# Kernel tuning notes

Hardware: AMD Instinct MI355X
Metric: run time of the kernel (lower is better)

Reference implementation:

```python
import jax, jax.numpy as jnp
import numpy as np

NUM_HEAD = 8
EMBED_DIM = 512


def setup_inputs() -> dict:
    key = jax.random.key(0)
    ks = jax.random.split(key, 9)
    B, N, D = 4, 2048, 512
    # xavier_uniform bound for square [D, D] weights
    bound = float(np.sqrt(6.0 / (D + EMBED_DIM)))
    return {
        "q": jax.random.normal(ks[0], (B, N, D), jnp.float32),
        "k": jax.random.normal(ks[1], (B, N, D), jnp.float32),
        "v": jax.random.normal(ks[2], (B, N, D), jnp.float32),
        "Wq": jax.random.uniform(ks[3], (D, EMBED_DIM), jnp.float32, -bound, bound),
        "Wk": jax.random.uniform(ks[4], (D, EMBED_DIM), jnp.float32, -bound, bound),
        "Wv": jax.random.uniform(ks[5], (D, EMBED_DIM), jnp.float32, -bound, bound),
        "bq": jnp.zeros((EMBED_DIM,), jnp.float32),
        "bk": jnp.zeros((EMBED_DIM,), jnp.float32),
        "bv": jnp.zeros((EMBED_DIM,), jnp.float32),
    }


def reference(q, k, v, Wq, Wk, Wv, bq, bk, bv):
    h = NUM_HEAD
    ch = EMBED_DIM // h
    B, N, _ = q.shape
    # linear projections
    Q = q @ Wq + bq  # [B, N, E]
    K = k @ Wk + bk
    V = v @ Wv + bv
    # split heads: b n (h ch) -> b h n ch
    Q = Q.reshape(B, N, h, ch).transpose(0, 2, 1, 3)
    K = K.reshape(B, N, h, ch).transpose(0, 2, 1, 3)
    V = V.reshape(B, N, h, ch).transpose(0, 2, 1, 3)
    scale = 1.0 / np.sqrt(ch).astype(np.float32)
    scores = jnp.einsum("bhqc,bhkc->bhqk", Q, K) * scale  # [B, h, N, N]
    attn = jax.nn.softmax(scores, axis=-1)
    out = jnp.einsum("bhqk,bhkc->bhqc", attn, V)  # [B, h, N, ch]
    # merge heads: b h n ch -> b n (h ch)
    return out.transpose(0, 2, 1, 3).reshape(B, N, EMBED_DIM)
```

## Files before the change

### kernel.cpp

```cpp
#include <hip/hip_runtime.h>
#include <hip/hip_bf16.h>
#include <cstdint>

#define B_ 4
#define N_ 2048
#define D_ 512
#define E_ 512
#define H_ 8
#define CH_ 64
#define M_ (B_*N_)

typedef __attribute__((ext_vector_type(8))) short bf16x8;
typedef __attribute__((ext_vector_type(4))) float f32x4;
typedef __attribute__((ext_vector_type(16))) float f32x16;
using u16 = unsigned short;
using u32 = unsigned int;

__device__ __forceinline__ u16 f2bf(float f) {
  union { __hip_bfloat16 h; u16 u; } cv;
  cv.h = __float2bfloat16(f);
  return cv.u;
}

__device__ __forceinline__ float fexp2(float x) {
#if __has_builtin(__builtin_amdgcn_exp2f)
  return __builtin_amdgcn_exp2f(x);
#else
  return exp2f(x);
#endif
}

__device__ __forceinline__ void async16(const void* g, void* l) {
  __builtin_amdgcn_global_load_lds(
      (__attribute__((address_space(1))) void*)(g),
      (__attribute__((address_space(3))) void*)(l),
      16, 0, 0);
}

__global__ void prep_w(const float* __restrict__ Wq, const float* __restrict__ Wk,
                       const float* __restrict__ Wv,
                       u16* __restrict__ tq, u16* __restrict__ tk, u16* __restrict__ tv) {
  int bid = blockIdx.x;
  int t = bid >> 10;
  const float* W = (t == 0) ? Wq : (t == 1 ? Wk : Wv);
  u16* T = (t == 0) ? tq : (t == 1 ? tk : tv);
  int idx = ((bid & 1023) << 8) + threadIdx.x;
  int e = idx >> 9, kd = idx & 511;
  T[idx] = f2bf(W[kd * E_ + e]);
}

#define GBM 128
#define GBN 128
#define GBK 64

__global__ __launch_bounds__(256) void proj_gemm(
    const float* __restrict__ xq, const float* __restrict__ xk, const float* __restrict__ xv,
    const u16* __restrict__ wtq, const u16* __restrict__ wtk, const u16* __restrict__ wtv,
    const float* __restrict__ bq, const float* __restrict__ bk, const float* __restrict__ bv,
    u16* __restrict__ Qp, u16* __restrict__ Kp, u16* __restrict__ Vp) {
  const int z = blockIdx.z;
  const float* X = (z == 0) ? xq : (z == 1 ? xk : xv);
  const u16* WT  = (z == 0) ? wtq : (z == 1 ? wtk : wtv);
  const float* bias = (z == 0) ? bq : (z == 1 ? bk : bv);
  u16* Out = (z == 0) ? Qp : (z == 1 ? Kp : Vp);
  const float scale = (z == 0) ? 0.18033688011112042f : 1.0f;
  const bool vlayout = (z == 2);

  __shared__ __align__(16) u16 As[GBM * GBK];
  __shared__ __align__(16) u16 Bs[GBN * GBK];

  const int tid = threadIdx.x;
  const int l = tid & 63, w = tid >> 6;
  const int wr = w >> 1, wc = w & 1;
  const int m0 = blockIdx.y * GBM;
  const int e0 = blockIdx.x * GBN;

  f32x4 acc[4][4] = {};

  for (int ks = 0; ks < D_ / GBK; ++ks) {
    const int k0 = ks * GBK;
#pragma unroll
    for (int i = 0; i < 4; ++i) {
      int o = i * 4096 + tid * 16;
      int row = o >> 7, colb = o & 127;
      int scol = colb ^ ((row & 7) << 4);
      async16((const char*)WT + ((size_t)(e0 + row) * D_ + k0) * 2 + scol, (char*)Bs + o);
    }
    float4 fa[4], fb_[4];
#pragma unroll
    for (int i = 0; i < 4; ++i) {
      int o = i * 4096 + tid * 16;
      int row = o >> 7, colb = o & 127;
      const char* src = (const char*)X + ((size_t)(m0 + row) * D_ + k0) * 4 + colb * 2;
      fa[i]  = *reinterpret_cast<const float4*>(src);
      fb_[i] = *reinterpret_cast<const float4*>(src + 16);
    }
#pragma unroll
    for (int i = 0; i < 4; ++i) {
      int o = i * 4096 + tid * 16;
      int row = o >> 7;
      union { u16 us[8]; bf16x8 v8; } cu;
      cu.us[0] = f2bf(fa[i].x); cu.us[1] = f2bf(fa[i].y);
      cu.us[2] = f2bf(fa[i].z); cu.us[3] = f2bf(fa[i].w);
      cu.us[4] = f2bf(fb_[i].x); cu.us[5] = f2bf(fb_[i].y);
      cu.us[6] = f2bf(fb_[i].z); cu.us[7] = f2bf(fb_[i].w);
      *reinterpret_cast<bf16x8*>((char*)As + (o ^ ((row & 7) << 4))) = cu.v8;
    }
    __syncthreads();
#pragma unroll
    for (int kk = 0; kk < 2; ++kk) {
      bf16x8 af[4], bfr[4];
#pragma unroll
      for (int m = 0; m < 4; ++m) {
        int row = wr * 64 + m * 16 + (l & 15);
        int addr = (row << 7) + kk * 64 + ((l >> 4) << 4);
        addr ^= (row & 7) << 4;
        af[m] = *reinterpret_cast<const bf16x8*>((const char*)As + addr);
      }
#pragma unroll
      for (int n = 0; n < 4; ++n) {
        int row = wc * 64 + n * 16 + (l & 15);
        int addr = (row << 7) + kk * 64 + ((l >> 4) << 4);
        addr ^= (row & 7) << 4;
        bfr[n] = *reinterpret_cast<const bf16x8*>((const char*)Bs + addr);
      }
#pragma unroll
      for (int m = 0; m < 4; ++m)
#pragma unroll
        for (int n = 0; n < 4; ++n)
          acc[m][n] = __builtin_amdgcn_mfma_f32_16x16x32_bf16(af[m], bfr[n], acc[m][n], 0, 0, 0);
    }
    __syncthreads();
  }

#pragma unroll
  for (int m = 0; m < 4; ++m) {
#pragma unroll
    for (int n = 0; n < 4; ++n) {
      int ge = e0 + wc * 64 + n * 16 + (l & 15);
      int h = ge >> 6, c = ge & 63;
      float bv_ = bias[ge];
      int gm0 = m0 + wr * 64 + m * 16 + ((l >> 4) << 2);
      int b = gm0 >> 11, nn0 = gm0 & 2047;
      if (vlayout) {
        short4 sv;
#pragma unroll
        for (int j = 0; j < 4; ++j)
          ((u16*)&sv)[j] = f2bf((acc[m][n][j] + bv_) * scale);
        int np = (((nn0 >> 2) ^ (nn0 >> 3)) & 1) ? (nn0 ^ 12) : nn0;
        *reinterpret_cast<short4*>(
            &Out[(((size_t)b * H_ + h) * CH_ + c) * N_ + np]) = sv;
      } else {
#pragma unroll
        for (int j = 0; j < 4; ++j) {
          u16 oval = f2bf((acc[m][n][j] + bv_) * scale);
          Out[((((size_t)b * H_ + h) * N_ + nn0 + j) << 6) + c] = oval;
        }
      }
    }
  }
}

#define QBLK 128
#define KVB 64
#define NTH 16

#define MFMA32(A, Bv, C) __builtin_amdgcn_mfma_f32_32x32x16_bf16((A), (Bv), (C), 0, 0, 0)

__global__ __launch_bounds__(512, 2) void attn_kernel(
    const u16* __restrict__ Qp, const u16* __restrict__ Kp, const u16* __restrict__ Vp,
    float* __restrict__ out) {
  __shared__ __align__(16) u16 Kb[2][2][KVB * 64];
  __shared__ __align__(16) u16 Vb[2][2][KVB * 64];

  const int tid = threadIdx.x;
  const int l = tid & 63, w = tid >> 6;
  const int wsub = w & 3, hf = w >> 2;
  const int qcol = l & 31, hi = l >> 5;

  const int beta = blockIdx.x;
  const int xcd = beta & 7, r = beta >> 3;
  const int bh = xcd * 4 + (r >> 4);
  const int qt = r & 15;

  const u16* Qh = Qp + (size_t)bh * N_ * CH_;
  const u16* Kh = Kp + (size_t)bh * N_ * CH_;
  const u16* Vh = Vp + (size_t)bh * CH_ * N_;
  const int bb = bh >> 3, hh = bh & 7;
  const int qrow = qt * QBLK + wsub * 32 + qcol;

  bf16x8 qf[4];
  {
    const u16* qptr = Qh + (size_t)qrow * CH_;
#pragma unroll
    for (int ks = 0; ks < 4; ++ks)
      qf[ks] = *reinterpret_cast<const bf16x8*>(qptr + ks * 16 + hi * 8);
  }

  f32x16 o0 = {}, o1 = {};
  float lrun = 0.f;

  const int rowA = qcol << 7;
  const int swz  = (l & 7) << 4;
  const int hi16 = hi << 4;
  const int st   = tid & 255;
  const int tb   = hf * NTH;

#define STAGE(BUF, KV) do {                                                      \
    _Pragma("unroll")                                                            \
    for (int i = 0; i < 2; ++i) {                                                \
      int o = i * 4096 + st * 16;                                                \
      int row = o >> 7, colb = o & 127;                                          \
      int scol = colb ^ ((row & 7) << 4);                                        \
      async16((const char*)Kh + ((size_t)((KV) + row) << 7) + scol,              \
              (char*)&Kb[BUF][hf][0] + o);                                       \
      async16((const char*)Vh + ((size_t)row * N_ + (KV)) * 2 + scol,            \
              (char*)&Vb[BUF][hf][0] + o);                                       \
    } } while (0)

#define TILE(BUF, TL) do {                                                       \
    if ((TL) + 1 < NTH) STAGE((BUF) ^ 1, (tb + (TL) + 1) * KVB);                 \
    f32x16 s0 = {}, s1 = {};                                                     \
    __builtin_amdgcn_s_setprio(1);                                               \
    _Pragma("unroll")                                                            \
    for (int ks = 0; ks < 4; ++ks) {                                             \
      int col = (ks * 32 + hi16) ^ swz;                                          \
      bf16x8 k0 = *reinterpret_cast<const bf16x8*>((const char*)&Kb[BUF][hf][0] + rowA + col);        \
      bf16x8 k1 = *reinterpret_cast<const bf16x8*>((const char*)&Kb[BUF][hf][0] + 4096 + rowA + col); \
      s0 = MFMA32(k0, qf[ks], s0);                                               \
      s1 = MFMA32(k1, qf[ks], s1);                                               \
    }                                                                            \
    __builtin_amdgcn_s_setprio(0);                                               \
    _Pragma("unroll")                                                            \
    for (int rr = 0; rr < 16; ++rr) { s0[rr] = fexp2(s0[rr]); s1[rr] = fexp2(s1[rr]); } \
    {                                                                            \
      float t0 = (s0[0] + s0[1]) + (s0[2] + s0[3]);                              \
      float t1 = (s0[4] + s0[5]) + (s0[6] + s0[7]);                              \
      float t2 = (s0[8] + s0[9]) + (s0[10] + s0[11]);                            \
      float t3 = (s0[12] + s0[13]) + (s0[14] + s0[15]);                          \
      float t4 = (s1[0] + s1[1]) + (s1[2] + s1[3]);                              \
      float t5 = (s1[4] + s1[5]) + (s1[6] + s1[7]);                              \
      float t6 = (s1[8] + s1[9]) + (s1[10] + s1[11]);                            \
      float t7 = (s1[12] + s1[13]) + (s1[14] + s1[15]);                          \
      float rsum = ((t0 + t1) + (t2 + t3)) + ((t4 + t5) + (t6 + t7));            \
      rsum += __shfl_xor(rsum, 32);                                              \
      lrun += rsum;                                                              \
    }                                                                            \
    __builtin_amdgcn_s_setprio(1);                                               \
    _Pragma("unroll")                                                            \
    for (int ks = 0; ks < 4; ++ks) {                                             \
      const f32x16& sv = (ks < 2) ? s0 : s1;                                     \
      const int b0 = 8 * (ks & 1);                                               \
      union { u16 us[8]; bf16x8 v8; } pu;                                        \
      _Pragma("unroll")                                                          \
      for (int j = 0; j < 8; ++j) pu.us[j] = f2bf(sv[b0 + j]);                   \
      int col = (ks * 32 + hi16) ^ swz;                                          \
      bf16x8 v0 = *reinterpret_cast<const bf16x8*>((const char*)&Vb[BUF][hf][0] + rowA + col);        \
      bf16x8 v1 = *reinterpret_cast<const bf16x8*>((const char*)&Vb[BUF][hf][0] + 4096 + rowA + col); \
      o0 = MFMA32(v0, pu.v8, o0);                                                \
      o1 = MFMA32(v1, pu.v8, o1);                                                \
    }                                                                            \
    __builtin_amdgcn_s_setprio(0);                                               \
    __syncthreads();                                                             \
  } while (0)

  STAGE(0, tb * KVB);
  __syncthreads();

  for (int tl = 0; tl < NTH; tl += 2) {
    TILE(0, tl);
    TILE(1, tl + 1);
  }

  float* shO = (float*)&Kb[0][0][0];
  float* shL = (float*)&Vb[0][0][0];
  if (hf == 1) {
    float* pb = shO + wsub * 2048 + l * 4;
#pragma unroll
    for (int c = 0; c < 4; ++c) {
      float4 s;
      s.x = o0[c * 4 + 0]; s.y = o0[c * 4 + 1];
      s.z = o0[c * 4 + 2]; s.w = o0[c * 4 + 3];
      *reinterpret_cast<float4*>(pb + c * 256) = s;
    }
#pragma unroll
    for (int c = 0; c < 4; ++c) {
      float4 s;
      s.x = o1[c * 4 + 0]; s.y = o1[c * 4 + 1];
      s.z = o1[c * 4 + 2]; s.w = o1[c * 4 + 3];
      *reinterpret_cast<float4*>(pb + (4 + c) * 256) = s;
    }
    shL[wsub * 64 + l] = lrun;
  }
  __syncthreads();
  if (hf == 0) {
    float inv = 1.0f / (lrun + shL[wsub * 64 + l]);
    const float* pb = shO + wsub * 2048 + l * 4;
    const size_t obase = ((size_t)bb * N_ + qrow) * E_ + hh * CH_;
#pragma unroll
    for (int c = 0; c < 4; ++c) {
      float4 p = *reinterpret_cast<const float4*>(pb + c * 256);
      float4 stv;
      stv.x = (o0[c * 4 + 0] + p.x) * inv;
      stv.y = (o0[c * 4 + 1] + p.y) * inv;
      stv.z = (o0[c * 4 + 2] + p.z) * inv;
      stv.w = (o0[c * 4 + 3] + p.w) * inv;
      *reinterpret_cast<float4*>(out + obase + 0 * 32 + c * 8 + hi * 4) = stv;
    }
#pragma unroll
    for (int c = 0; c < 4; ++c) {
      float4 p = *reinterpret_cast<const float4*>(pb + (4 + c) * 256);
      float4 stv;
      stv.x = (o1[c * 4 + 0] + p.x) * inv;
      stv.y = (o1[c * 4 + 1] + p.y) * inv;
      stv.z = (o1[c * 4 + 2] + p.z) * inv;
      stv.w = (o1[c * 4 + 3] + p.w) * inv;
      *reinterpret_cast<float4*>(out + obase + 1 * 32 + c * 8 + hi * 4) = stv;
    }
  }
#undef STAGE
#undef TILE
}

extern "C" void kernel_launch(void* const* d_in, const int* in_sizes, int n_in,
                              void* d_out, int out_size, void* d_ws, size_t ws_size,
                              hipStream_t stream) {
  const float* q  = (const float*)d_in[0];
  const float* k  = (const float*)d_in[1];
  const float* v  = (const float*)d_in[2];
  const float* Wq = (const float*)d_in[3];
  const float* Wk = (const float*)d_in[4];
  const float* Wv = (const float*)d_in[5];
  const float* bq = (const float*)d_in[6];
  const float* bk = (const float*)d_in[7];
  const float* bv = (const float*)d_in[8];
  float* out = (float*)d_out;

  u16* wtq = (u16*)d_ws;
  u16* wtk = wtq + (size_t)D_ * E_;
  u16* wtv = wtk + (size_t)D_ * E_;
  u16* Qp  = wtv + (size_t)D_ * E_;
  u16* Kp  = Qp + (size_t)M_ * E_;
  u16* Vp  = Kp + (size_t)M_ * E_;

  prep_w<<<3072, 256, 0, stream>>>(Wq, Wk, Wv, wtq, wtk, wtv);
  proj_gemm<<<dim3(E_ / GBN, M_ / GBM, 3), 256, 0, stream>>>(
      q, k, v, wtq, wtk, wtv, bq, bk, bv, Qp, Kp, Vp);
  attn_kernel<<<512, 512, 0, stream>>>(Qp, Kp, Vp, out);
}
```

Before: 90.28 us.

## Pre-convert activations to bf16 and async-load both GEMM operands into LDS

The prep kernel now also converts the q/k/v fp32 activations to bf16 in workspace. The projection GEMM then loads both A and B tiles with direct global-to-LDS async copies instead of doing fp32 register loads and in-loop conversion. This removes the repeated fp32 reads of the activations across N-blocks and the conversion ALU work in the GEMM loop. In exchange it adds a full extra memory pass and 24 MB of workspace for the bf16 copies.

```diff
diff --git a/kernel.cpp b/kernel.cpp
--- a/kernel.cpp
+++ b/kernel.cpp
@@ -37,16 +37,31 @@
       16, 0, 0);
 }
 
-__global__ void prep_w(const float* __restrict__ Wq, const float* __restrict__ Wk,
-                       const float* __restrict__ Wv,
-                       u16* __restrict__ tq, u16* __restrict__ tk, u16* __restrict__ tv) {
+__global__ void prep(const float* __restrict__ q, const float* __restrict__ k,
+                     const float* __restrict__ v,
+                     const float* __restrict__ Wq, const float* __restrict__ Wk,
+                     const float* __restrict__ Wv,
+                     u16* __restrict__ qb, u16* __restrict__ kb, u16* __restrict__ vb,
+                     u16* __restrict__ tq, u16* __restrict__ tk, u16* __restrict__ tv) {
   int bid = blockIdx.x;
-  int t = bid >> 10;
-  const float* W = (t == 0) ? Wq : (t == 1 ? Wk : Wv);
-  u16* T = (t == 0) ? tq : (t == 1 ? tk : tv);
-  int idx = ((bid & 1023) << 8) + threadIdx.x;
-  int e = idx >> 9, kd = idx & 511;
-  T[idx] = f2bf(W[kd * E_ + e]);
+  if (bid < 12288) {
+    int t = bid >> 12;
+    const float* in = (t == 0) ? q : (t == 1 ? k : v);
+    u16* outp = (t == 0) ? qb : (t == 1 ? kb : vb);
+    int i = ((bid & 4095) << 8) + threadIdx.x;
+    float4 f = reinterpret_cast<const float4*>(in)[i];
+    ushort4 o;
+    o.x = f2bf(f.x); o.y = f2bf(f.y); o.z = f2bf(f.z); o.w = f2bf(f.w);
+    reinterpret_cast<ushort4*>(outp)[i] = o;
+  } else {
+    bid -= 12288;
+    int t = bid >> 10;
+    const float* W = (t == 0) ? Wq : (t == 1 ? Wk : Wv);
+    u16* T = (t == 0) ? tq : (t == 1 ? tk : tv);
+    int idx = ((bid & 1023) << 8) + threadIdx.x;
+    int e = idx >> 9, kd = idx & 511;
+    T[idx] = f2bf(W[kd * E_ + e]);
+  }
 }
 
 #define GBM 128
@@ -54,13 +69,13 @@
 #define GBK 64
 
 __global__ __launch_bounds__(256) void proj_gemm(
-    const float* __restrict__ xq, const float* __restrict__ xk, const float* __restrict__ xv,
+    const u16* __restrict__ xq, const u16* __restrict__ xk, const u16* __restrict__ xv,
     const u16* __restrict__ wtq, const u16* __restrict__ wtk, const u16* __restrict__ wtv,
     const float* __restrict__ bq, const float* __restrict__ bk, const float* __restrict__ bv,
     u16* __restrict__ Qp, u16* __restrict__ Kp, u16* __restrict__ Vp) {
   const int z = blockIdx.z;
-  const float* X = (z == 0) ? xq : (z == 1 ? xk : xv);
-  const u16* WT  = (z == 0) ? wtq : (z == 1 ? wtk : wtv);
+  const u16* X  = (z == 0) ? xq : (z == 1 ? xk : xv);
+  const u16* WT = (z == 0) ? wtq : (z == 1 ? wtk : wtv);
   const float* bias = (z == 0) ? bq : (z == 1 ? bk : bv);
   u16* Out = (z == 0) ? Qp : (z == 1 ? Kp : Vp);
   const float scale = (z == 0) ? 0.18033688011112042f : 1.0f;
@@ -84,27 +99,8 @@
       int o = i * 4096 + tid * 16;
       int row = o >> 7, colb = o & 127;
       int scol = colb ^ ((row & 7) << 4);
+      async16((const char*)X  + ((size_t)(m0 + row) * D_ + k0) * 2 + scol, (char*)As + o);
       async16((const char*)WT + ((size_t)(e0 + row) * D_ + k0) * 2 + scol, (char*)Bs + o);
-    }
-    float4 fa[4], fb_[4];
-#pragma unroll
-    for (int i = 0; i < 4; ++i) {
-      int o = i * 4096 + tid * 16;
-      int row = o >> 7, colb = o & 127;
-      const char* src = (const char*)X + ((size_t)(m0 + row) * D_ + k0) * 4 + colb * 2;
-      fa[i]  = *reinterpret_cast<const float4*>(src);
-      fb_[i] = *reinterpret_cast<const float4*>(src + 16);
-    }
-#pragma unroll
-    for (int i = 0; i < 4; ++i) {
-      int o = i * 4096 + tid * 16;
-      int row = o >> 7;
-      union { u16 us[8]; bf16x8 v8; } cu;
-      cu.us[0] = f2bf(fa[i].x); cu.us[1] = f2bf(fa[i].y);
-      cu.us[2] = f2bf(fa[i].z); cu.us[3] = f2bf(fa[i].w);
-      cu.us[4] = f2bf(fb_[i].x); cu.us[5] = f2bf(fb_[i].y);
-      cu.us[6] = f2bf(fb_[i].z); cu.us[7] = f2bf(fb_[i].w);
-      *reinterpret_cast<bf16x8*>((char*)As + (o ^ ((row & 7) << 4))) = cu.v8;
     }
     __syncthreads();
 #pragma unroll
@@ -342,9 +338,12 @@
   u16* Qp  = wtv + (size_t)D_ * E_;
   u16* Kp  = Qp + (size_t)M_ * E_;
   u16* Vp  = Kp + (size_t)M_ * E_;
-
-  prep_w<<<3072, 256, 0, stream>>>(Wq, Wk, Wv, wtq, wtk, wtv);
+  u16* qb  = Vp + (size_t)M_ * E_;
+  u16* kb  = qb + (size_t)M_ * D_;
+  u16* vb  = kb + (size_t)M_ * D_;
+
+  prep<<<15360, 256, 0, stream>>>(q, k, v, Wq, Wk, Wv, qb, kb, vb, wtq, wtk, wtv);
   proj_gemm<<<dim3(E_ / GBN, M_ / GBM, 3), 256, 0, stream>>>(
-      q, k, v, wtq, wtk, wtv, bq, bk, bv, Qp, Kp, Vp);
+      qb, kb, vb, wtq, wtk, wtv, bq, bk, bv, Qp, Kp, Vp);
   attn_kernel<<<512, 512, 0, stream>>>(Qp, Kp, Vp, out);
 }
```

After: 87.90 us. 2.6% less time.
